# Performance work log

Measured on AMD Instinct MI355X. Metric: run time of the kernel, lower is better.

Reference implementation:

```python
import jax, jax.numpy as jnp
import numpy as np

B = 131072      # batch
IN = 1024       # input_dim
H = 384         # hidden[0]
L = 128         # latent_dim = hidden[1]
K = 32          # slots_k
R = 2           # top_r
TAU = 0.7


def setup_inputs() -> dict:
    key = jax.random.key(0)
    ks = jax.random.split(key, 8)
    s = 0.02
    f32 = jnp.float32
    return {
        "x":  jax.random.normal(ks[0], (B, IN), f32),
        "w1": jax.random.normal(ks[1], (IN, H), f32) * s,
        "b1": jnp.zeros((H,), f32),
        "w2": jax.random.normal(ks[2], (H, L), f32) * s,
        "b2": jnp.zeros((L,), f32),
        "mk": jax.random.normal(ks[3], (K, L), f32) * s,  # memory_keys
        "mv": jax.random.normal(ks[4], (K, L), f32) * s,  # memory_values
        "w3": jax.random.normal(ks[5], (2 * L, H), f32) * s,
        "b3": jnp.zeros((H,), f32),
        "w4": jax.random.normal(ks[6], (H, 1), f32) * s,
        "b4": jnp.zeros((1,), f32),
    }


def reference(x, w1, b1, w2, b2, mk, mv, w3, b3, w4, b4):
    # block_a: Linear -> GELU -> (Dropout=id in eval) -> Linear -> GELU
    z = jax.nn.gelu(x @ w1 + b1, approximate=False)
    z = jax.nn.gelu(z @ w2 + b2, approximate=False)          # [B, L]

    # top-r slot attention over memory bank
    logits = (z @ mk.T) / TAU                                 # [B, K]
    _, idx = jax.lax.top_k(logits, R)                         # [B, R]
    keep = jax.nn.one_hot(idx, K, dtype=logits.dtype).sum(-2) > 0  # [B, K] bool
    masked = jnp.where(keep, logits, -jnp.inf)
    attn = jax.nn.softmax(masked, axis=-1)                    # [B, K]
    mem = attn @ mv                                           # [B, L]

    fused = jnp.concatenate([z, mem], axis=-1)                # [B, 2L]

    # default head: Linear -> GELU -> Linear(.,1)
    h = jax.nn.gelu(fused @ w3 + b3, approximate=False)
    logit = (h @ w4 + b4)[..., 0]                             # [B]
    return jax.nn.sigmoid(logit)
```

## Files before the change

kernel.cpp:

```cpp
#include <hip/hip_runtime.h>

#define BATCH   131072
#define INDIM   1024
#define BM      64
#define BDIM    512
#define NBLK    (BATCH / BM)

#define WT0_OFF  0
#define WT1_OFF  24576
#define XT0_OFF  49152
#define XT1_OFF  53248
#define Z1_OFF   0
#define W2T0_OFF 50176
#define W2T1_OFF 58368
#define FZ_OFF   0
#define LG_OFF   33792
#define RP_OFF   33792
#define W3T_OFF  42240
#define CB_OFF   68096
#define B1S_OFF  (CB_OFF)
#define B2S_OFF  (CB_OFF + 1536)
#define B3S_OFF  (CB_OFF + 2048)
#define W4S_OFF  (CB_OFF + 3584)
#define MKS_OFF  (CB_OFF + 5120)
#define SMEM_BYTES 81920

typedef unsigned short u16;
typedef u16    u16x8  __attribute__((ext_vector_type(8)));
typedef u16    u16x4  __attribute__((ext_vector_type(4)));
typedef __bf16 bf16x8 __attribute__((ext_vector_type(8)));
typedef __bf16 bf16x4 __attribute__((ext_vector_type(4)));
typedef float  f32x4  __attribute__((ext_vector_type(4)));

__device__ __forceinline__ u16 f2bf(float f) {
  unsigned u = __float_as_uint(f);
  u += 0x7FFFu + ((u >> 16) & 1u);
  return (u16)(u >> 16);
}

__device__ __forceinline__ float gelu_exact(float v) {
  return 0.5f * v * (1.0f + erff(v * 0.70710678118654752440f));
}

__device__ __forceinline__ f32x4 mfma16(u16x8 a, u16x8 b, f32x4 c) {
  return __builtin_amdgcn_mfma_f32_16x16x32_bf16(
      __builtin_bit_cast(bf16x8, a), __builtin_bit_cast(bf16x8, b), c, 0, 0, 0);
}

__device__ __forceinline__ u16x8 cvt8(float4 a, float4 b) {
  bf16x8 r;
  r[0]=(__bf16)a.x; r[1]=(__bf16)a.y; r[2]=(__bf16)a.z; r[3]=(__bf16)a.w;
  r[4]=(__bf16)b.x; r[5]=(__bf16)b.y; r[6]=(__bf16)b.z; r[7]=(__bf16)b.w;
  return __builtin_bit_cast(u16x8, r);
}
__device__ __forceinline__ u16x4 cvt4(float4 a) {
  bf16x4 r;
  r[0]=(__bf16)a.x; r[1]=(__bf16)a.y; r[2]=(__bf16)a.z; r[3]=(__bf16)a.w;
  return __builtin_bit_cast(u16x4, r);
}

typedef __attribute__((address_space(3))) unsigned int       lds_u32;
typedef __attribute__((address_space(1))) const unsigned int glb_u32;
__device__ __forceinline__ void gload16(const void* g, void* l) {
  __builtin_amdgcn_global_load_lds((glb_u32*)g, (lds_u32*)l, 16, 0, 0);
}

#define FENCE_SCHED __builtin_amdgcn_sched_barrier(0)
#define WAIT_LGKM0 do { asm volatile("s_waitcnt lgkmcnt(0)" ::: "memory"); FENCE_SCHED; } while (0)
#define WAIT_VMN(N) do { \
  asm volatile("s_waitcnt vmcnt(" #N ")" ::: "memory"); FENCE_SCHED; } while (0)
#define BARRIER_VMN(N) do { \
  asm volatile("s_waitcnt vmcnt(" #N ") lgkmcnt(0)" ::: "memory"); \
  __builtin_amdgcn_s_barrier(); FENCE_SCHED; } while (0)

__global__ void prep_kernel(const float* __restrict__ w1, const float* __restrict__ w2,
                            const float* __restrict__ w3, u16* __restrict__ w1s,
                            u16* __restrict__ w2s, u16* __restrict__ w3s) {
  int i = blockIdx.x * 256 + threadIdx.x;
  if (i < 393216) {
    int t = i / 12288, p = i % 12288;
    int r = p >> 5, q = p & 31, cp = q >> 3, o = q & 7;
    int k = t * 32 + ((cp ^ ((r >> 1) & 3)) << 3) + o;
    w1s[i] = f2bf(w1[k * 384 + r]);
  } else if (i < 442368) {
    int j = i - 393216;
    int t = j / 4096, p = j % 4096;
    int r = p >> 5, q = p & 31, cp = q >> 3, o = q & 7;
    int k = t * 32 + ((cp ^ ((r >> 1) & 3)) << 3) + o;
    w2s[j] = f2bf(w2[k * 128 + r]);
  } else if (i < 540672) {
    int j = i - 442368;
    int t = j / 12288, p = j % 12288;
    int r = p >> 5, q = p & 31, cp = q >> 3, o = q & 7;
    int k = t * 32 + ((cp ^ ((r >> 1) & 3)) << 3) + o;
    w3s[j] = f2bf(w3[k * 384 + r]);
  }
}

__global__ __launch_bounds__(BDIM, 4) void fused_kernel(
    const float* __restrict__ x,  const u16* __restrict__ w1s,
    const float* __restrict__ b1, const u16* __restrict__ w2s,
    const float* __restrict__ b2, const float* __restrict__ mkw,
    const float* __restrict__ mvw, const u16* __restrict__ w3s,
    const float* __restrict__ b3, const float* __restrict__ w4,
    const float* __restrict__ b4, float* __restrict__ out) {
  extern __shared__ char smem[];
  u16*   z1  = (u16*)(smem + Z1_OFF);
  u16*   fz  = (u16*)(smem + FZ_OFF);
  float* lgs = (float*)(smem + LG_OFF);
  u16*   w3t = (u16*)(smem + W3T_OFF);
  float* b1s = (float*)(smem + B1S_OFF);
  float* b2s = (float*)(smem + B2S_OFF);
  float* b3s = (float*)(smem + B3S_OFF);
  float* w4s = (float*)(smem + W4S_OFF);
  u16*   mks = (u16*)(smem + MKS_OFF);
  float* rowpart = (float*)(smem + RP_OFF);

  const int tid  = threadIdx.x;
  const int lane = tid & 63;
  const int wid  = tid >> 6;
  const int l15  = lane & 15;
  const int g    = lane >> 4;
  const int xsw8 = (g ^ ((l15 >> 1) & 3)) * 8;
  const int row0 = blockIdx.x * BM;
  const int wstrip = wid * 1536;
  const int wrow   = wid * 48;

  {
    const u16* ws = w1s + wstrip + lane * 8;
    u16* wd = (u16*)(smem + WT0_OFF) + wstrip;
    gload16(ws, wd); gload16(ws + 512, wd + 512); gload16(ws + 1024, wd + 1024);
  }
  const int xrow = tid >> 3, xq = tid & 7;
  const float* xp = x + (long)(row0 + xrow) * INDIM + xq * 4;
  const int xpub = xrow * 32 + (((xq >> 1) ^ ((xrow >> 1) & 3)) << 3) + (xq & 1) * 4;
  float4 xr = *(const float4*)xp;

  for (int i = tid; i < 384; i += BDIM) b1s[i] = b1[i];
  if (tid < 128) b2s[tid] = b2[tid];
  for (int i = tid; i < 384; i += BDIM) b3s[i] = b3[i];
  for (int i = tid; i < 384; i += BDIM) w4s[i] = w4[i];
  {
    int r = tid >> 4, cc = (tid & 15) * 8;
    const float4* p = (const float4*)(mkw + r * 128 + cc);
    float4 a = p[0], b = p[1];
    *(u16x8*)(mks + r * 136 + cc) = cvt8(a, b);
  }
  *(u16x4*)((u16*)(smem + XT0_OFF) + xpub) = cvt4(xr);
  {
    const u16* ws = w1s + 12288 + wstrip + lane * 8;
    u16* wd = (u16*)(smem + WT1_OFF) + wstrip;
    gload16(ws, wd); gload16(ws + 512, wd + 512); gload16(ws + 1024, wd + 1024);
  }
  xr = *(const float4*)(xp + 32);
  BARRIER_VMN(4);

  f32x4 acc[4][3];
  #pragma unroll
  for (int m = 0; m < 4; ++m)
    #pragma unroll
    for (int n = 0; n < 3; ++n) acc[m][n] = (f32x4){0.f, 0.f, 0.f, 0.f};

#define G1_STEP(KT, XB, WB, XN, DO_PF, LAST_VMN)                                 \
  do {                                                                           \
    const u16* xb = (const u16*)(smem + (XB));                                   \
    const u16* wb = (const u16*)(smem + (WB));                                   \
    u16x8 af[4], bfr[3];                                                         \
    _Pragma("unroll")                                                            \
    for (int m = 0; m < 4; ++m)                                                  \
      af[m] = *(const u16x8*)(xb + (m * 16 + l15) * 32 + xsw8);                  \
    _Pragma("unroll")                                                            \
    for (int n = 0; n < 3; ++n)                                                  \
      bfr[n] = *(const u16x8*)(wb + (wrow + n * 16 + l15) * 32 + xsw8);          \
    WAIT_LGKM0;                                                                  \
    if (DO_PF) {                                                                 \
      const u16* ws = w1s + ((KT) + 2) * 12288 + wstrip + lane * 8;              \
      u16* wd = (u16*)(smem + (WB)) + wstrip;                                    \
      gload16(ws, wd); gload16(ws + 512, wd + 512); gload16(ws + 1024, wd + 1024); \
      *(u16x4*)((u16*)(smem + (XN)) + xpub) = cvt4(xr);                          \
      xr = *(const float4*)(xp + ((KT) + 2) * 32);                               \
    }                                                                            \
    _Pragma("unroll")                                                            \
    for (int m = 0; m < 4; ++m)                                                  \
      _Pragma("unroll")                                                          \
      for (int n = 0; n < 3; ++n) acc[m][n] = mfma16(af[m], bfr[n], acc[m][n]);  \
  } while (0)

  for (int kt = 0; kt < 30; kt += 2) {
    G1_STEP(kt,     XT0_OFF, WT0_OFF, XT1_OFF, 1, 4);
    BARRIER_VMN(4);
    G1_STEP(kt + 1, XT1_OFF, WT1_OFF, XT0_OFF, 1, 4);
    BARRIER_VMN(4);
  }
  {
    const u16* xb = (const u16*)(smem + XT0_OFF);
    const u16* wb = (const u16*)(smem + WT0_OFF);
    u16x8 af[4], bfr[3];
    #pragma unroll
    for (int m = 0; m < 4; ++m) af[m] = *(const u16x8*)(xb + (m * 16 + l15) * 32 + xsw8);
    #pragma unroll
    for (int n = 0; n < 3; ++n) bfr[n] = *(const u16x8*)(wb + (wrow + n * 16 + l15) * 32 + xsw8);
    WAIT_LGKM0;
    *(u16x4*)((u16*)(smem + XT1_OFF) + xpub) = cvt4(xr);
    #pragma unroll
    for (int m = 0; m < 4; ++m)
      #pragma unroll
      for (int n = 0; n < 3; ++n) acc[m][n] = mfma16(af[m], bfr[n], acc[m][n]);
    BARRIER_VMN(0);
  }
  {
    const u16* xb = (const u16*)(smem + XT1_OFF);
    const u16* wb = (const u16*)(smem + WT1_OFF);
    u16x8 af[4], bfr[3];
    #pragma unroll
    for (int m = 0; m < 4; ++m) af[m] = *(const u16x8*)(xb + (m * 16 + l15) * 32 + xsw8);
    #pragma unroll
    for (int n = 0; n < 3; ++n) bfr[n] = *(const u16x8*)(wb + (wrow + n * 16 + l15) * 32 + xsw8);
    WAIT_LGKM0;
    #pragma unroll
    for (int m = 0; m < 4; ++m)
      #pragma unroll
      for (int n = 0; n < 3; ++n) acc[m][n] = mfma16(af[m], bfr[n], acc[m][n]);
  }
  __syncthreads();

  {
    const u16* s2 = w2s + wid * 512 + lane * 8;
    gload16(s2, (u16*)(smem + W2T0_OFF) + wid * 512);
    const u16* s2b = w2s + 4096 + wid * 512 + lane * 8;
    gload16(s2b, (u16*)(smem + W2T1_OFF) + wid * 512);
  }
  #pragma unroll
  for (int m = 0; m < 4; ++m) {
    #pragma unroll
    for (int n = 0; n < 3; ++n) {
      int col = wrow + n * 16 + l15;
      float bias = b1s[col];
      #pragma unroll
      for (int j = 0; j < 4; ++j)
        z1[(m * 16 + g * 4 + j) * 392 + col] = f2bf(gelu_exact(acc[m][n][j] + bias));
    }
  }
  __syncthreads();

  f32x4 acc2[4];
  #pragma unroll
  for (int m = 0; m < 4; ++m) acc2[m] = (f32x4){0.f, 0.f, 0.f, 0.f};
  for (int kt = 0; kt < 11; ++kt) {
    WAIT_VMN(1);
    const u16* wbuf = (const u16*)(smem + W2T0_OFF + (kt & 1) * 8192);
    u16x8 a2f[4], b2f;
    #pragma unroll
    for (int m = 0; m < 4; ++m)
      a2f[m] = *(const u16x8*)(z1 + (m * 16 + l15) * 392 + kt * 32 + g * 8);
    b2f = *(const u16x8*)(wbuf + (wid * 16 + l15) * 32 + xsw8);
    WAIT_LGKM0;
    if (kt < 10) {
      const u16* s2 = w2s + (kt + 2) * 4096 + wid * 512 + lane * 8;
      gload16(s2, (u16*)(smem + W2T0_OFF + (kt & 1) * 8192) + wid * 512);
    }
    #pragma unroll
    for (int m = 0; m < 4; ++m) acc2[m] = mfma16(a2f[m], b2f, acc2[m]);
  }
  {
    WAIT_VMN(0);
    const u16* wbuf = (const u16*)(smem + W2T1_OFF);
    u16x8 a2f[4], b2f;
    #pragma unroll
    for (int m = 0; m < 4; ++m)
      a2f[m] = *(const u16x8*)(z1 + (m * 16 + l15) * 392 + 352 + g * 8);
    b2f = *(const u16x8*)(wbuf + (wid * 16 + l15) * 32 + xsw8);
    WAIT_LGKM0;
    #pragma unroll
    for (int m = 0; m < 4; ++m) acc2[m] = mfma16(a2f[m], b2f, acc2[m]);
  }
  __syncthreads();

  {
    const u16* s3 = w3s + wstrip + lane * 8;
    u16* d3 = w3t + wstrip;
    gload16(s3, d3); gload16(s3 + 512, d3 + 512); gload16(s3 + 1024, d3 + 1024);
  }
  #pragma unroll
  for (int m = 0; m < 4; ++m) {
    int col = wid * 16 + l15;
    float bias = b2s[col];
    #pragma unroll
    for (int j = 0; j < 4; ++j)
      fz[(m * 16 + g * 4 + j) * 264 + col] = f2bf(gelu_exact(acc2[m][j] + bias));
  }
  __syncthreads();

  if (wid < 4) {
    f32x4 accl[2] = {(f32x4){0,0,0,0}, (f32x4){0,0,0,0}};
    const int alo = (wid * 16 + l15) * 264 + g * 8;
    const int blo = l15 * 136 + g * 8;
    #pragma unroll
    for (int ks = 0; ks < 4; ++ks) {
      u16x8 a  = *(const u16x8*)(fz + alo + ks * 32);
      u16x8 q0 = *(const u16x8*)(mks + blo + ks * 32);
      u16x8 q1 = *(const u16x8*)(mks + blo + 2176 + ks * 32);
      accl[0] = mfma16(a, q0, accl[0]);
      accl[1] = mfma16(a, q1, accl[1]);
    }
    #pragma unroll
    for (int n = 0; n < 2; ++n)
      #pragma unroll
      for (int j = 0; j < 4; ++j)
        lgs[(wid * 16 + g * 4 + j) * 33 + n * 16 + l15] = accl[n][j] * (1.0f / 0.7f);
  }
  __syncthreads();

  {
    int row = tid >> 3, q = tid & 7;
    const float* lp = lgs + row * 33 + q * 4;
    float m1 = -3.4e38f, m2 = -3.4e38f; int i1 = -1, i2 = -1;
    #pragma unroll
    for (int s = 0; s < 4; ++s) {
      float v = lp[s]; int idx = q * 4 + s;
      if (v > m1) { m2 = m1; i2 = i1; m1 = v; i1 = idx; }
      else if (v > m2) { m2 = v; i2 = idx; }
    }
    #pragma unroll
    for (int d = 1; d <= 4; d <<= 1) {
      float om1 = __shfl_xor(m1, d); int oi1 = __shfl_xor(i1, d);
      float om2 = __shfl_xor(m2, d); int oi2 = __shfl_xor(i2, d);
      bool take = (om1 > m1) || (om1 == m1 && oi1 < i1);
      if (take) {
        float nm2; int ni2;
        if (m1 > om2 || (m1 == om2 && i1 < oi2)) { nm2 = m1; ni2 = i1; }
        else { nm2 = om2; ni2 = oi2; }
        m1 = om1; i1 = oi1; m2 = nm2; i2 = ni2;
      } else {
        if (om1 > m2 || (om1 == m2 && oi1 < i2)) { m2 = om1; i2 = oi1; }
      }
    }
    float a1 = 1.0f / (1.0f + expf(m2 - m1));
    float a2 = 1.0f - a1;
    const float4* v1 = (const float4*)(mvw + i1 * 128 + q * 16);
    const float4* v2 = (const float4*)(mvw + i2 * 128 + q * 16);
    float4 pa = v1[0], pb = v1[1], ra = v2[0], rb = v2[1];
    u16x8 o;
    o[0]=f2bf(a1*pa.x+a2*ra.x); o[1]=f2bf(a1*pa.y+a2*ra.y);
    o[2]=f2bf(a1*pa.z+a2*ra.z); o[3]=f2bf(a1*pa.w+a2*ra.w);
    o[4]=f2bf(a1*pb.x+a2*rb.x); o[5]=f2bf(a1*pb.y+a2*rb.y);
    o[6]=f2bf(a1*pb.z+a2*rb.z); o[7]=f2bf(a1*pb.w+a2*rb.w);
    *(u16x8*)(fz + row * 264 + 128 + q * 16) = o;
    pa = v1[2]; pb = v1[3]; ra = v2[2]; rb = v2[3];
    o[0]=f2bf(a1*pa.x+a2*ra.x); o[1]=f2bf(a1*pa.y+a2*ra.y);
    o[2]=f2bf(a1*pa.z+a2*ra.z); o[3]=f2bf(a1*pa.w+a2*ra.w);
    o[4]=f2bf(a1*pb.x+a2*rb.x); o[5]=f2bf(a1*pb.y+a2*rb.y);
    o[6]=f2bf(a1*pb.z+a2*rb.z); o[7]=f2bf(a1*pb.w+a2*rb.w);
    *(u16x8*)(fz + row * 264 + 128 + q * 16 + 8) = o;
  }
  __syncthreads();

  f32x4 acc3[4][3];
  #pragma unroll
  for (int m = 0; m < 4; ++m)
    #pragma unroll
    for (int n = 0; n < 3; ++n) acc3[m][n] = (f32x4){0.f, 0.f, 0.f, 0.f};
  for (int kt = 0; kt < 8; ++kt) {
    WAIT_VMN(0);
    u16x8 a3f[4], b3f[3];
    #pragma unroll
    for (int m = 0; m < 4; ++m)
      a3f[m] = *(const u16x8*)(fz + (m * 16 + l15) * 264 + kt * 32 + g * 8);
    #pragma unroll
    for (int n = 0; n < 3; ++n)
      b3f[n] = *(const u16x8*)(w3t + (wrow + n * 16 + l15) * 32 + xsw8);
    WAIT_LGKM0;
    if (kt < 7) {
      const u16* s3 = w3s + (kt + 1) * 12288 + wstrip + lane * 8;
      u16* d3 = w3t + wstrip;
      gload16(s3, d3); gload16(s3 + 512, d3 + 512); gload16(s3 + 1024, d3 + 1024);
    }
    #pragma unroll
    for (int m = 0; m < 4; ++m)
      #pragma unroll
      for (int n = 0; n < 3; ++n) acc3[m][n] = mfma16(a3f[m], b3f[n], acc3[m][n]);
  }

  #pragma unroll
  for (int m = 0; m < 4; ++m) {
    float s0 = 0.f, s1 = 0.f, s2 = 0.f, s3 = 0.f;
    #pragma unroll
    for (int n = 0; n < 3; ++n) {
      int col = wrow + n * 16 + l15;
      float bias = b3s[col], wv = w4s[col];
      s0 += gelu_exact(acc3[m][n][0] + bias) * wv;
      s1 += gelu_exact(acc3[m][n][1] + bias) * wv;
      s2 += gelu_exact(acc3[m][n][2] + bias) * wv;
      s3 += gelu_exact(acc3[m][n][3] + bias) * wv;
    }
    #pragma unroll
    for (int d = 1; d < 16; d <<= 1) {
      s0 += __shfl_xor(s0, d); s1 += __shfl_xor(s1, d);
      s2 += __shfl_xor(s2, d); s3 += __shfl_xor(s3, d);
    }
    if (l15 == 0) {
      int rb = m * 16 + g * 4;
      rowpart[(rb + 0) * 8 + wid] = s0;
      rowpart[(rb + 1) * 8 + wid] = s1;
      rowpart[(rb + 2) * 8 + wid] = s2;
      rowpart[(rb + 3) * 8 + wid] = s3;
    }
  }
  __syncthreads();
  if (tid < BM) {
    float lg = b4[0];
    #pragma unroll
    for (int w = 0; w < 8; ++w) lg += rowpart[tid * 8 + w];
    out[row0 + tid] = 1.0f / (1.0f + expf(-lg));
  }
}

extern "C" void kernel_launch(void* const* d_in, const int* in_sizes, int n_in,
                              void* d_out, int out_size, void* d_ws, size_t ws_size,
                              hipStream_t stream) {
  const float* x  = (const float*)d_in[0];
  const float* w1 = (const float*)d_in[1];
  const float* b1 = (const float*)d_in[2];
  const float* w2 = (const float*)d_in[3];
  const float* b2 = (const float*)d_in[4];
  const float* mk = (const float*)d_in[5];
  const float* mv = (const float*)d_in[6];
  const float* w3 = (const float*)d_in[7];
  const float* b3 = (const float*)d_in[8];
  const float* w4 = (const float*)d_in[9];
  const float* b4 = (const float*)d_in[10];

  u16* w1s = (u16*)d_ws;
  u16* w2s = w1s + 393216;
  u16* w3s = w1s + 442368;

  prep_kernel<<<2112, 256, 0, stream>>>(w1, w2, w3, w1s, w2s, w3s);

  (void)hipFuncSetAttribute(reinterpret_cast<const void*>(fused_kernel),
                            hipFuncAttributeMaxDynamicSharedMemorySize, SMEM_BYTES);
  fused_kernel<<<NBLK, BDIM, SMEM_BYTES, stream>>>(x, w1s, b1, w2s, b2, mk, mv, w3s,
                                                   b3, w4, b4, (float*)d_out);
}
```

Before: 284.3 us.

## Restructure fused MLP kernel: K=64 tiles, swapped MFMA operands, tanh GELU

Layer 1 now runs 16 K-steps of 64 with a single W1 LDS buffer and a double-buffered x tile, instead of 32 steps of 32 with both double-buffered. The prep swizzle is updated to match. MFMA operands are swapped so each lane holds four consecutive columns, which allows vectorized bias loads and packed bf16 stores. Top-2 selection now runs directly in registers, removing the logits LDS round trip and one barrier. The exact erf GELU is replaced by a tanh/exp2 approximation using hardware exp and rcp, which trades some accuracy for fewer instructions.

```diff
diff --git a/kernel.cpp b/kernel.cpp
--- a/kernel.cpp
+++ b/kernel.cpp
@@ -6,24 +6,22 @@
 #define BDIM    512
 #define NBLK    (BATCH / BM)
 
-#define WT0_OFF  0
-#define WT1_OFF  24576
+#define WT_OFF   0
 #define XT0_OFF  49152
-#define XT1_OFF  53248
+#define XT1_OFF  57344
 #define Z1_OFF   0
 #define W2T0_OFF 50176
 #define W2T1_OFF 58368
 #define FZ_OFF   0
-#define LG_OFF   33792
 #define RP_OFF   33792
 #define W3T_OFF  42240
-#define CB_OFF   68096
+#define CB_OFF   66816
 #define B1S_OFF  (CB_OFF)
 #define B2S_OFF  (CB_OFF + 1536)
 #define B3S_OFF  (CB_OFF + 2048)
 #define W4S_OFF  (CB_OFF + 3584)
 #define MKS_OFF  (CB_OFF + 5120)
-#define SMEM_BYTES 81920
+#define SMEM_BYTES (CB_OFF + 13824)
 
 typedef unsigned short u16;
 typedef u16    u16x8  __attribute__((ext_vector_type(8)));
@@ -38,8 +36,11 @@
   return (u16)(u >> 16);
 }
 
-__device__ __forceinline__ float gelu_exact(float v) {
-  return 0.5f * v * (1.0f + erff(v * 0.70710678118654752440f));
+__device__ __forceinline__ float gelu_fast(float v) {
+  float t = v * v;
+  float u = v * fmaf(t, 0.0356774081f, 0.7978845608f);
+  float e = __builtin_amdgcn_exp2f(u * -2.885390082f);
+  return v * __builtin_amdgcn_rcpf(1.0f + e);
 }
 
 __device__ __forceinline__ f32x4 mfma16(u16x8 a, u16x8 b, f32x4 c) {
@@ -67,10 +68,9 @@
 
 #define FENCE_SCHED __builtin_amdgcn_sched_barrier(0)
 #define WAIT_LGKM0 do { asm volatile("s_waitcnt lgkmcnt(0)" ::: "memory"); FENCE_SCHED; } while (0)
-#define WAIT_VMN(N) do { \
-  asm volatile("s_waitcnt vmcnt(" #N ")" ::: "memory"); FENCE_SCHED; } while (0)
-#define BARRIER_VMN(N) do { \
-  asm volatile("s_waitcnt vmcnt(" #N ") lgkmcnt(0)" ::: "memory"); \
+#define WAIT_VMN(N) do { asm volatile("s_waitcnt vmcnt(" #N ")" ::: "memory"); FENCE_SCHED; } while (0)
+#define BARRIER_LGKM do { \
+  asm volatile("s_waitcnt lgkmcnt(0)" ::: "memory"); \
   __builtin_amdgcn_s_barrier(); FENCE_SCHED; } while (0)
 
 __global__ void prep_kernel(const float* __restrict__ w1, const float* __restrict__ w2,
@@ -78,9 +78,9 @@
                             u16* __restrict__ w2s, u16* __restrict__ w3s) {
   int i = blockIdx.x * 256 + threadIdx.x;
   if (i < 393216) {
-    int t = i / 12288, p = i % 12288;
-    int r = p >> 5, q = p & 31, cp = q >> 3, o = q & 7;
-    int k = t * 32 + ((cp ^ ((r >> 1) & 3)) << 3) + o;
+    int t = i / 24576, p = i % 24576;
+    int r = p >> 6, q = p & 63, cp = q >> 3, o = q & 7;
+    int k = t * 64 + ((cp ^ (r & 7)) << 3) + o;
     w1s[i] = f2bf(w1[k * 384 + r]);
   } else if (i < 442368) {
     int j = i - 393216;
@@ -107,7 +107,6 @@
   extern __shared__ char smem[];
   u16*   z1  = (u16*)(smem + Z1_OFF);
   u16*   fz  = (u16*)(smem + FZ_OFF);
-  float* lgs = (float*)(smem + LG_OFF);
   u16*   w3t = (u16*)(smem + W3T_OFF);
   float* b1s = (float*)(smem + B1S_OFF);
   float* b2s = (float*)(smem + B2S_OFF);
@@ -121,39 +120,36 @@
   const int wid  = tid >> 6;
   const int l15  = lane & 15;
   const int g    = lane >> 4;
-  const int xsw8 = (g ^ ((l15 >> 1) & 3)) * 8;
+  const int swz8 = l15 & 7;
+  const int swz4 = (l15 >> 1) & 3;
   const int row0 = blockIdx.x * BM;
-  const int wstrip = wid * 1536;
-  const int wrow   = wid * 48;
+  const int wrow = wid * 48;
+  const int wstrip = wid * 3072;
 
   {
     const u16* ws = w1s + wstrip + lane * 8;
-    u16* wd = (u16*)(smem + WT0_OFF) + wstrip;
-    gload16(ws, wd); gload16(ws + 512, wd + 512); gload16(ws + 1024, wd + 1024);
-  }
-  const int xrow = tid >> 3, xq = tid & 7;
-  const float* xp = x + (long)(row0 + xrow) * INDIM + xq * 4;
-  const int xpub = xrow * 32 + (((xq >> 1) ^ ((xrow >> 1) & 3)) << 3) + (xq & 1) * 4;
-  float4 xr = *(const float4*)xp;
-
-  for (int i = tid; i < 384; i += BDIM) b1s[i] = b1[i];
+    u16* wd = (u16*)(smem + WT_OFF) + wstrip;
+    #pragma unroll
+    for (int i = 0; i < 6; ++i) gload16(ws + i * 512, wd + i * 512);
+  }
+  FENCE_SCHED;
+  const int xrow = tid >> 3, xoct = tid & 7;
+  const float* xp = x + (long)(row0 + xrow) * INDIM + xoct * 8;
+  const int xdst = xrow * 64 + ((xoct ^ (xrow & 7)) << 3);
+  float4 xa = *(const float4*)xp, xb = *(const float4*)(xp + 4);
+
+  if (tid < 384) b1s[tid] = b1[tid];
   if (tid < 128) b2s[tid] = b2[tid];
-  for (int i = tid; i < 384; i += BDIM) b3s[i] = b3[i];
-  for (int i = tid; i < 384; i += BDIM) w4s[i] = w4[i];
+  if (tid < 384) b3s[tid] = b3[tid];
+  if (tid < 384) w4s[tid] = w4[tid];
   {
     int r = tid >> 4, cc = (tid & 15) * 8;
     const float4* p = (const float4*)(mkw + r * 128 + cc);
-    float4 a = p[0], b = p[1];
-    *(u16x8*)(mks + r * 136 + cc) = cvt8(a, b);
-  }
-  *(u16x4*)((u16*)(smem + XT0_OFF) + xpub) = cvt4(xr);
-  {
-    const u16* ws = w1s + 12288 + wstrip + lane * 8;
-    u16* wd = (u16*)(smem + WT1_OFF) + wstrip;
-    gload16(ws, wd); gload16(ws + 512, wd + 512); gload16(ws + 1024, wd + 1024);
-  }
-  xr = *(const float4*)(xp + 32);
-  BARRIER_VMN(4);
+    *(u16x8*)(mks + r * 136 + cc) = cvt8(p[0], p[1]);
+  }
+  *(u16x8*)((u16*)(smem + XT0_OFF) + xdst) = cvt8(xa, xb);
+  { const float* p = xp + 64; xa = *(const float4*)p; xb = *(const float4*)(p + 4); }
+  BARRIER_LGKM;
 
   f32x4 acc[4][3];
   #pragma unroll
@@ -161,68 +157,46 @@
     #pragma unroll
     for (int n = 0; n < 3; ++n) acc[m][n] = (f32x4){0.f, 0.f, 0.f, 0.f};
 
-#define G1_STEP(KT, XB, WB, XN, DO_PF, LAST_VMN)                                 \
-  do {                                                                           \
-    const u16* xb = (const u16*)(smem + (XB));                                   \
-    const u16* wb = (const u16*)(smem + (WB));                                   \
-    u16x8 af[4], bfr[3];                                                         \
-    _Pragma("unroll")                                                            \
-    for (int m = 0; m < 4; ++m)                                                  \
-      af[m] = *(const u16x8*)(xb + (m * 16 + l15) * 32 + xsw8);                  \
-    _Pragma("unroll")                                                            \
-    for (int n = 0; n < 3; ++n)                                                  \
-      bfr[n] = *(const u16x8*)(wb + (wrow + n * 16 + l15) * 32 + xsw8);          \
-    WAIT_LGKM0;                                                                  \
-    if (DO_PF) {                                                                 \
-      const u16* ws = w1s + ((KT) + 2) * 12288 + wstrip + lane * 8;              \
-      u16* wd = (u16*)(smem + (WB)) + wstrip;                                    \
-      gload16(ws, wd); gload16(ws + 512, wd + 512); gload16(ws + 1024, wd + 1024); \
-      *(u16x4*)((u16*)(smem + (XN)) + xpub) = cvt4(xr);                          \
-      xr = *(const float4*)(xp + ((KT) + 2) * 32);                               \
-    }                                                                            \
-    _Pragma("unroll")                                                            \
-    for (int m = 0; m < 4; ++m)                                                  \
-      _Pragma("unroll")                                                          \
-      for (int n = 0; n < 3; ++n) acc[m][n] = mfma16(af[m], bfr[n], acc[m][n]);  \
-  } while (0)
-
-  for (int kt = 0; kt < 30; kt += 2) {
-    G1_STEP(kt,     XT0_OFF, WT0_OFF, XT1_OFF, 1, 4);
-    BARRIER_VMN(4);
-    G1_STEP(kt + 1, XT1_OFF, WT1_OFF, XT0_OFF, 1, 4);
-    BARRIER_VMN(4);
-  }
-  {
-    const u16* xb = (const u16*)(smem + XT0_OFF);
-    const u16* wb = (const u16*)(smem + WT0_OFF);
+  const u16* wtb = (const u16*)(smem + WT_OFF);
+  for (int kt = 0; kt < 16; ++kt) {
+    if (kt < 15) { WAIT_VMN(2); } else { WAIT_VMN(0); }
+    const u16* xtb = (const u16*)(smem + ((kt & 1) ? XT1_OFF : XT0_OFF));
     u16x8 af[4], bfr[3];
-    #pragma unroll
-    for (int m = 0; m < 4; ++m) af[m] = *(const u16x8*)(xb + (m * 16 + l15) * 32 + xsw8);
-    #pragma unroll
-    for (int n = 0; n < 3; ++n) bfr[n] = *(const u16x8*)(wb + (wrow + n * 16 + l15) * 32 + xsw8);
+    const int c0 = (g ^ swz8) * 8;
+    #pragma unroll
+    for (int m = 0; m < 4; ++m) af[m] = *(const u16x8*)(xtb + (m * 16 + l15) * 64 + c0);
+    #pragma unroll
+    for (int n = 0; n < 3; ++n) bfr[n] = *(const u16x8*)(wtb + (wrow + n * 16 + l15) * 64 + c0);
+    #pragma unroll
+    for (int m = 0; m < 4; ++m)
+      #pragma unroll
+      for (int n = 0; n < 3; ++n) acc[m][n] = mfma16(bfr[n], af[m], acc[m][n]);
+    const int c1 = ((g + 4) ^ swz8) * 8;
+    #pragma unroll
+    for (int m = 0; m < 4; ++m) af[m] = *(const u16x8*)(xtb + (m * 16 + l15) * 64 + c1);
+    #pragma unroll
+    for (int n = 0; n < 3; ++n) bfr[n] = *(const u16x8*)(wtb + (wrow + n * 16 + l15) * 64 + c1);
     WAIT_LGKM0;
-    *(u16x4*)((u16*)(smem + XT1_OFF) + xpub) = cvt4(xr);
-    #pragma unroll
-    for (int m = 0; m < 4; ++m)
-      #pragma unroll
-      for (int n = 0; n < 3; ++n) acc[m][n] = mfma16(af[m], bfr[n], acc[m][n]);
-    BARRIER_VMN(0);
-  }
-  {
-    const u16* xb = (const u16*)(smem + XT1_OFF);
-    const u16* wb = (const u16*)(smem + WT1_OFF);
-    u16x8 af[4], bfr[3];
-    #pragma unroll
-    for (int m = 0; m < 4; ++m) af[m] = *(const u16x8*)(xb + (m * 16 + l15) * 32 + xsw8);
-    #pragma unroll
-    for (int n = 0; n < 3; ++n) bfr[n] = *(const u16x8*)(wb + (wrow + n * 16 + l15) * 32 + xsw8);
-    WAIT_LGKM0;
-    #pragma unroll
-    for (int m = 0; m < 4; ++m)
-      #pragma unroll
-      for (int n = 0; n < 3; ++n) acc[m][n] = mfma16(af[m], bfr[n], acc[m][n]);
-  }
-  __syncthreads();
+    if (kt < 15) {
+      const u16* ws = w1s + (kt + 1) * 24576 + wstrip + lane * 8;
+      u16* wd = (u16*)(smem + WT_OFF) + wstrip;
+      #pragma unroll
+      for (int i = 0; i < 6; ++i) gload16(ws + i * 512, wd + i * 512);
+      FENCE_SCHED;
+      u16* xn = (u16*)(smem + ((kt & 1) ? XT0_OFF : XT1_OFF));
+      *(u16x8*)(xn + xdst) = cvt8(xa, xb);
+      if (kt < 14) {
+        const float* p = xp + (kt + 2) * 64;
+        xa = *(const float4*)p; xb = *(const float4*)(p + 4);
+      }
+      BARRIER_LGKM;
+    }
+    #pragma unroll
+    for (int m = 0; m < 4; ++m)
+      #pragma unroll
+      for (int n = 0; n < 3; ++n) acc[m][n] = mfma16(bfr[n], af[m], acc[m][n]);
+  }
+  BARRIER_LGKM;
 
   {
     const u16* s2 = w2s + wid * 512 + lane * 8;
@@ -234,95 +208,75 @@
   for (int m = 0; m < 4; ++m) {
     #pragma unroll
     for (int n = 0; n < 3; ++n) {
-      int col = wrow + n * 16 + l15;
-      float bias = b1s[col];
-      #pragma unroll
-      for (int j = 0; j < 4; ++j)
-        z1[(m * 16 + g * 4 + j) * 392 + col] = f2bf(gelu_exact(acc[m][n][j] + bias));
-    }
-  }
-  __syncthreads();
+      int col = wrow + n * 16 + g * 4;
+      float4 bv = *(const float4*)(b1s + col);
+      f32x4 a = acc[m][n];
+      float4 gv = {gelu_fast(a[0] + bv.x), gelu_fast(a[1] + bv.y),
+                   gelu_fast(a[2] + bv.z), gelu_fast(a[3] + bv.w)};
+      *(u16x4*)(z1 + (m * 16 + l15) * 392 + col) = cvt4(gv);
+    }
+  }
+  BARRIER_LGKM;
 
   f32x4 acc2[4];
   #pragma unroll
   for (int m = 0; m < 4; ++m) acc2[m] = (f32x4){0.f, 0.f, 0.f, 0.f};
-  for (int kt = 0; kt < 11; ++kt) {
-    WAIT_VMN(1);
-    const u16* wbuf = (const u16*)(smem + W2T0_OFF + (kt & 1) * 8192);
-    u16x8 a2f[4], b2f;
+  for (int kt = 0; kt < 12; ++kt) {
+    if (kt < 10) { WAIT_VMN(1); } else { WAIT_VMN(0); }
+    const u16* wb = (const u16*)(smem + ((kt & 1) ? W2T1_OFF : W2T0_OFF));
+    u16x8 a2f[4];
     #pragma unroll
     for (int m = 0; m < 4; ++m)
       a2f[m] = *(const u16x8*)(z1 + (m * 16 + l15) * 392 + kt * 32 + g * 8);
-    b2f = *(const u16x8*)(wbuf + (wid * 16 + l15) * 32 + xsw8);
+    u16x8 b2f = *(const u16x8*)(wb + (wid * 16 + l15) * 32 + (g ^ swz4) * 8);
     WAIT_LGKM0;
     if (kt < 10) {
       const u16* s2 = w2s + (kt + 2) * 4096 + wid * 512 + lane * 8;
-      gload16(s2, (u16*)(smem + W2T0_OFF + (kt & 1) * 8192) + wid * 512);
-    }
-    #pragma unroll
-    for (int m = 0; m < 4; ++m) acc2[m] = mfma16(a2f[m], b2f, acc2[m]);
-  }
+      gload16(s2, (u16*)(smem + ((kt & 1) ? W2T1_OFF : W2T0_OFF)) + wid * 512);
+    }
+    #pragma unroll
+    for (int m = 0; m < 4; ++m) acc2[m] = mfma16(b2f, a2f[m], acc2[m]);
+  }
+  BARRIER_LGKM;
+
   {
-    WAIT_VMN(0);
-    const u16* wbuf = (const u16*)(smem + W2T1_OFF);
-    u16x8 a2f[4], b2f;
-    #pragma unroll
-    for (int m = 0; m < 4; ++m)
-      a2f[m] = *(const u16x8*)(z1 + (m * 16 + l15) * 392 + 352 + g * 8);
-    b2f = *(const u16x8*)(wbuf + (wid * 16 + l15) * 32 + xsw8);
-    WAIT_LGKM0;
-    #pragma unroll
-    for (int m = 0; m < 4; ++m) acc2[m] = mfma16(a2f[m], b2f, acc2[m]);
-  }
-  __syncthreads();
-
-  {
-    const u16* s3 = w3s + wstrip + lane * 8;
-    u16* d3 = w3t + wstrip;
+    const u16* s3 = w3s + wid * 1536 + lane * 8;
+    u16* d3 = w3t + wid * 1536;
     gload16(s3, d3); gload16(s3 + 512, d3 + 512); gload16(s3 + 1024, d3 + 1024);
   }
   #pragma unroll
   for (int m = 0; m < 4; ++m) {
-    int col = wid * 16 + l15;
-    float bias = b2s[col];
-    #pragma unroll
-    for (int j = 0; j < 4; ++j)
-      fz[(m * 16 + g * 4 + j) * 264 + col] = f2bf(gelu_exact(acc2[m][j] + bias));
-  }
-  __syncthreads();
+    int col = wid * 16 + g * 4;
+    float4 bv = *(const float4*)(b2s + col);
+    f32x4 a = acc2[m];
+    float4 gv = {gelu_fast(a[0] + bv.x), gelu_fast(a[1] + bv.y),
+                 gelu_fast(a[2] + bv.z), gelu_fast(a[3] + bv.w)};
+    *(u16x4*)(fz + (m * 16 + l15) * 264 + col) = cvt4(gv);
+  }
+  BARRIER_LGKM;
 
   if (wid < 4) {
+    const int wr = wid * 16 + l15;
     f32x4 accl[2] = {(f32x4){0,0,0,0}, (f32x4){0,0,0,0}};
-    const int alo = (wid * 16 + l15) * 264 + g * 8;
-    const int blo = l15 * 136 + g * 8;
     #pragma unroll
     for (int ks = 0; ks < 4; ++ks) {
-      u16x8 a  = *(const u16x8*)(fz + alo + ks * 32);
-      u16x8 q0 = *(const u16x8*)(mks + blo + ks * 32);
-      u16x8 q1 = *(const u16x8*)(mks + blo + 2176 + ks * 32);
-      accl[0] = mfma16(a, q0, accl[0]);
-      accl[1] = mfma16(a, q1, accl[1]);
-    }
+      u16x8 afz = *(const u16x8*)(fz + wr * 264 + ks * 32 + g * 8);
+      u16x8 k0  = *(const u16x8*)(mks + l15 * 136 + ks * 32 + g * 8);
+      u16x8 k1  = *(const u16x8*)(mks + (16 + l15) * 136 + ks * 32 + g * 8);
+      accl[0] = mfma16(k0, afz, accl[0]);
+      accl[1] = mfma16(k1, afz, accl[1]);
+    }
+    float m1 = -3.4e38f, m2 = -3.4e38f; int i1 = -1, i2 = -1;
     #pragma unroll
     for (int n = 0; n < 2; ++n)
       #pragma unroll
-      for (int j = 0; j < 4; ++j)
-        lgs[(wid * 16 + g * 4 + j) * 33 + n * 16 + l15] = accl[n][j] * (1.0f / 0.7f);
-  }
-  __syncthreads();
-
-  {
-    int row = tid >> 3, q = tid & 7;
-    const float* lp = lgs + row * 33 + q * 4;
-    float m1 = -3.4e38f, m2 = -3.4e38f; int i1 = -1, i2 = -1;
-    #pragma unroll
-    for (int s = 0; s < 4; ++s) {
-      float v = lp[s]; int idx = q * 4 + s;
-      if (v > m1) { m2 = m1; i2 = i1; m1 = v; i1 = idx; }
-      else if (v > m2) { m2 = v; i2 = idx; }
-    }
-    #pragma unroll
-    for (int d = 1; d <= 4; d <<= 1) {
+      for (int j = 0; j < 4; ++j) {
+        float v = accl[n][j]; int idx = n * 16 + g * 4 + j;
+        if (v > m1) { m2 = m1; i2 = i1; m1 = v; i1 = idx; }
+        else if (v > m2) { m2 = v; i2 = idx; }
+      }
+    #pragma unroll
+    for (int d = 16; d <= 32; d <<= 1) {
       float om1 = __shfl_xor(m1, d); int oi1 = __shfl_xor(i1, d);
       float om2 = __shfl_xor(m2, d); int oi2 = __shfl_xor(i2, d);
       bool take = (om1 > m1) || (om1 == m1 && oi1 < i1);
@@ -335,25 +289,21 @@
         if (om1 > m2 || (om1 == m2 && oi1 < i2)) { m2 = om1; i2 = oi1; }
       }
     }
-    float a1 = 1.0f / (1.0f + expf(m2 - m1));
+    float a1 = __builtin_amdgcn_rcpf(
+        1.0f + __builtin_amdgcn_exp2f((m2 - m1) * (1.44269504f / 0.7f)));
     float a2 = 1.0f - a1;
-    const float4* v1 = (const float4*)(mvw + i1 * 128 + q * 16);
-    const float4* v2 = (const float4*)(mvw + i2 * 128 + q * 16);
-    float4 pa = v1[0], pb = v1[1], ra = v2[0], rb = v2[1];
-    u16x8 o;
-    o[0]=f2bf(a1*pa.x+a2*ra.x); o[1]=f2bf(a1*pa.y+a2*ra.y);
-    o[2]=f2bf(a1*pa.z+a2*ra.z); o[3]=f2bf(a1*pa.w+a2*ra.w);
-    o[4]=f2bf(a1*pb.x+a2*rb.x); o[5]=f2bf(a1*pb.y+a2*rb.y);
-    o[6]=f2bf(a1*pb.z+a2*rb.z); o[7]=f2bf(a1*pb.w+a2*rb.w);
-    *(u16x8*)(fz + row * 264 + 128 + q * 16) = o;
-    pa = v1[2]; pb = v1[3]; ra = v2[2]; rb = v2[3];
-    o[0]=f2bf(a1*pa.x+a2*ra.x); o[1]=f2bf(a1*pa.y+a2*ra.y);
-    o[2]=f2bf(a1*pa.z+a2*ra.z); o[3]=f2bf(a1*pa.w+a2*ra.w);
-    o[4]=f2bf(a1*pb.x+a2*rb.x); o[5]=f2bf(a1*pb.y+a2*rb.y);
-    o[6]=f2bf(a1*pb.z+a2*rb.z); o[7]=f2bf(a1*pb.w+a2*rb.w);
-    *(u16x8*)(fz + row * 264 + 128 + q * 16 + 8) = o;
-  }
-  __syncthreads();
+    const float* v1 = mvw + i1 * 128 + g * 32;
+    const float* v2 = mvw + i2 * 128 + g * 32;
+    #pragma unroll
+    for (int c = 0; c < 4; ++c) {
+      float4 A0 = *(const float4*)(v1 + c * 8), A1 = *(const float4*)(v1 + c * 8 + 4);
+      float4 B0 = *(const float4*)(v2 + c * 8), B1 = *(const float4*)(v2 + c * 8 + 4);
+      float4 r0 = {a1*A0.x + a2*B0.x, a1*A0.y + a2*B0.y, a1*A0.z + a2*B0.z, a1*A0.w + a2*B0.w};
+      float4 r1 = {a1*A1.x + a2*B1.x, a1*A1.y + a2*B1.y, a1*A1.z + a2*B1.z, a1*A1.w + a2*B1.w};
+      *(u16x8*)(fz + wr * 264 + 128 + g * 32 + c * 8) = cvt8(r0, r1);
+    }
+  }
+  BARRIER_LGKM;
 
   f32x4 acc3[4][3];
   #pragma unroll
@@ -368,50 +318,41 @@
       a3f[m] = *(const u16x8*)(fz + (m * 16 + l15) * 264 + kt * 32 + g * 8);
     #pragma unroll
     for (int n = 0; n < 3; ++n)
-      b3f[n] = *(const u16x8*)(w3t + (wrow + n * 16 + l15) * 32 + xsw8);
+      b3f[n] = *(const u16x8*)(w3t + (wrow + n * 16 + l15) * 32 + (g ^ swz4) * 8);
     WAIT_LGKM0;
     if (kt < 7) {
-      const u16* s3 = w3s + (kt + 1) * 12288 + wstrip + lane * 8;
-      u16* d3 = w3t + wstrip;
+      const u16* s3 = w3s + (kt + 1) * 12288 + wid * 1536 + lane * 8;
+      u16* d3 = w3t + wid * 1536;
       gload16(s3, d3); gload16(s3 + 512, d3 + 512); gload16(s3 + 1024, d3 + 1024);
     }
     #pragma unroll
     for (int m = 0; m < 4; ++m)
       #pragma unroll
-      for (int n = 0; n < 3; ++n) acc3[m][n] = mfma16(a3f[m], b3f[n], acc3[m][n]);
+      for (int n = 0; n < 3; ++n) acc3[m][n] = mfma16(b3f[n], a3f[m], acc3[m][n]);
   }
 
   #pragma unroll
   for (int m = 0; m < 4; ++m) {
-    float s0 = 0.f, s1 = 0.f, s2 = 0.f, s3 = 0.f;
+    float s = 0.f;
     #pragma unroll
     for (int n = 0; n < 3; ++n) {
-      int col = wrow + n * 16 + l15;
-      float bias = b3s[col], wv = w4s[col];
-      s0 += gelu_exact(acc3[m][n][0] + bias) * wv;
-      s1 += gelu_exact(acc3[m][n][1] + bias) * wv;
-      s2 += gelu_exact(acc3[m][n][2] + bias) * wv;
-      s3 += gelu_exact(acc3[m][n][3] + bias) * wv;
-    }
-    #pragma unroll
-    for (int d = 1; d < 16; d <<= 1) {
-      s0 += __shfl_xor(s0, d); s1 += __shfl_xor(s1, d);
-      s2 += __shfl_xor(s2, d); s3 += __shfl_xor(s3, d);
-    }
-    if (l15 == 0) {
-      int rb = m * 16 + g * 4;
-      rowpart[(rb + 0) * 8 + wid] = s0;
-      rowpart[(rb + 1) * 8 + wid] = s1;
-      rowpart[(rb + 2) * 8 + wid] = s2;
-      rowpart[(rb + 3) * 8 + wid] = s3;
-    }
-  }
-  __syncthreads();
+      int col = wrow + n * 16 + g * 4;
+      float4 bv = *(const float4*)(b3s + col);
+      float4 wv = *(const float4*)(w4s + col);
+      f32x4 a = acc3[m][n];
+      s += gelu_fast(a[0] + bv.x) * wv.x + gelu_fast(a[1] + bv.y) * wv.y +
+           gelu_fast(a[2] + bv.z) * wv.z + gelu_fast(a[3] + bv.w) * wv.w;
+    }
+    s += __shfl_xor(s, 16);
+    s += __shfl_xor(s, 32);
+    if (lane < 16) rowpart[(m * 16 + l15) * 8 + wid] = s;
+  }
+  BARRIER_LGKM;
   if (tid < BM) {
-    float lg = b4[0];
-    #pragma unroll
-    for (int w = 0; w < 8; ++w) lg += rowpart[tid * 8 + w];
-    out[row0 + tid] = 1.0f / (1.0f + expf(-lg));
+    const float4* rp = (const float4*)(rowpart + tid * 8);
+    float4 p0 = rp[0], p1 = rp[1];
+    float lg = b4[0] + p0.x + p0.y + p0.z + p0.w + p1.x + p1.y + p1.z + p1.w;
+    out[row0 + tid] = __builtin_amdgcn_rcpf(1.0f + __builtin_amdgcn_exp2f(-lg * 1.44269504f));
   }
 }
 
```

After: 232.0 us (median of 2 runs). 18.4% less time.
